# Kernel tuning notes

Measured on AMD Instinct MI355X. Metric: run time of the kernel, lower is better.

## Reference

```python
import jax, jax.numpy as jnp
import numpy as np

B = 16384      # batch
IN = 151       # input dim (layer_widths[0])
HID = 200      # RBF out_features (layer_widths[1])
CENT = 2000    # layer_centres[0]


def setup_inputs() -> dict:
    key = jax.random.key(0)
    ks = jax.random.split(key, 6)
    x = jax.random.normal(ks[0], (B, IN), dtype=jnp.float32)
    # RBF params per reset_parameters: centres ~ N(0, 0.01), sigmas = 2
    centres = 0.01 * jax.random.normal(ks[1], (HID, IN), dtype=jnp.float32)
    sigmas = jnp.full((HID,), 2.0, dtype=jnp.float32)
    # Linear layers (torch layout: weight is (out, in))
    w1 = jax.random.normal(ks[2], (CENT, HID), dtype=jnp.float32) / jnp.sqrt(jnp.float32(HID))
    b1 = jnp.zeros((CENT,), dtype=jnp.float32)
    # small scale so exp() stays well-conditioned
    w2 = 0.001 * jax.random.normal(ks[3], (CENT, CENT), dtype=jnp.float32)
    b2 = jnp.zeros((CENT,), dtype=jnp.float32)
    # kernel matrix (151, 2000); positive so Ehat[:, 0] > 0
    kern = jax.random.uniform(ks[4], (IN, CENT), dtype=jnp.float32)
    return {"x": x, "centres": centres, "sigmas": sigmas,
            "w1": w1, "b1": b1, "w2": w2, "b2": b2, "kern": kern}


def reference(x, centres, sigmas, w1, b1, w2, b2, kern):
    # RBF layer: distances_ij = ||x_i - c_j||_2 * sigma_j ; phi = exp(-distances^2)
    # exp(-(sqrt(d2)*sigma)^2) == exp(-d2 * sigma^2), so we skip the sqrt and the
    # (B, CENT, IN) expand tensor entirely.
    x2 = jnp.sum(x * x, axis=1, keepdims=True)            # (B, 1)
    c2 = jnp.sum(centres * centres, axis=1)[None, :]      # (1, HID)
    d2 = jnp.maximum(x2 + c2 - 2.0 * (x @ centres.T), 0.0)  # (B, HID)
    phi = jnp.exp(-d2 * (sigmas * sigmas)[None, :])       # (B, HID)

    h = jax.nn.relu(phi @ w1.T + b1)                      # (B, CENT)
    out = jnp.exp(h @ w2.T + b2)                          # (B, CENT)

    Ehat = out @ kern.T                                   # (B, IN)  == matmul(kern, out.T).T
    Rhat = out / Ehat[:, :1]                              # divide by correction term Ehat[:, 0]
    Ehat2 = Rhat @ kern.T                                 # (B, IN)
    return (Ehat2, Rhat, Ehat2, Rhat, x)
```

## Files before the change

kernel.cpp:

```cpp
#include <hip/hip_runtime.h>

#define BDIM 16384
#define IN_D 151
#define HID_D 200
#define CENT_D 2000

#define INP 192
#define HIDP 256
#define CENTP 2048
#define KERN_R 192

using bf16x8 = __attribute__((ext_vector_type(8))) short;
using f32x4  = __attribute__((ext_vector_type(4))) float;
using f4     = __attribute__((ext_vector_type(4))) float;
using us4    = __attribute__((ext_vector_type(4))) unsigned short;
using us8    = __attribute__((ext_vector_type(8))) unsigned short;
using i32x4  = __attribute__((ext_vector_type(4))) int;
using i32x8  = __attribute__((ext_vector_type(8))) int;

__device__ __forceinline__ unsigned short f2bf(float f) {
  unsigned u = __builtin_bit_cast(unsigned, f);
  u += 0x7FFFu + ((u >> 16) & 1u);
  return (unsigned short)(u >> 16);
}
__device__ __forceinline__ float bf2f(unsigned short h) {
  unsigned u = ((unsigned)h) << 16;
  return __builtin_bit_cast(float, u);
}
__device__ __forceinline__ unsigned char f2fp8(float f) {
  return (unsigned char)(__builtin_amdgcn_cvt_pk_fp8_f32(f, f, 0, false) & 0xFF);
}

typedef __attribute__((address_space(1))) const unsigned int guint;
typedef __attribute__((address_space(3))) unsigned int luint;
__device__ __forceinline__ void g2l16(const void* g, void* l) {
  __builtin_amdgcn_global_load_lds((guint*)g, (luint*)l, 16, 0, 0);
}

struct G0Args {
  const unsigned short* A;
  const unsigned short* B;
  const float* x2; const float* c2; const float* sg2;
  unsigned char* o8;
};

__global__ __launch_bounds__(256) void gemm_phi(G0Args p) {
  __shared__ __align__(16) short As[64 * 64];
  __shared__ __align__(16) short Bs[128 * 64];
  const int tid  = threadIdx.x;
  const int lane = tid & 63;
  const int w    = tid >> 6;
  const int wr   = w >> 1, wc = w & 1;
  const int lr   = lane & 15;
  const int tm = blockIdx.x, tn = blockIdx.y;
  f32x4 acc[2][4] = {};

  const unsigned short* Ag = p.A + (size_t)tm * 64 * INP;
  const unsigned short* Bg = p.B + (size_t)tn * 128 * INP;

  int rowa[2], cola[2], lda_[2];
#pragma unroll
  for (int i = 0; i < 2; i++) {
    int cc = i * 256 + tid;
    rowa[i] = cc >> 3;
    cola[i] = ((cc & 7) ^ (rowa[i] & 7)) * 8;
    lda_[i] = cc * 8;
  }
  int rowb[4], colb[4], ldb_[4];
#pragma unroll
  for (int i = 0; i < 4; i++) {
    int cc = i * 256 + tid;
    rowb[i] = cc >> 3;
    colb[i] = ((cc & 7) ^ (rowb[i] & 7)) * 8;
    ldb_[i] = cc * 8;
  }

  for (int k0 = 0; k0 < INP; k0 += 64) {
    __syncthreads();
#pragma unroll
    for (int i = 0; i < 2; i++)
      g2l16(Ag + (size_t)rowa[i] * INP + k0 + cola[i], &As[lda_[i]]);
#pragma unroll
    for (int i = 0; i < 4; i++)
      g2l16(Bg + (size_t)rowb[i] * INP + k0 + colb[i], &Bs[ldb_[i]]);
    __syncthreads();
#pragma unroll
    for (int ks = 0; ks < 2; ks++) {
      bf16x8 af[2], bfr[4];
#pragma unroll
      for (int m = 0; m < 2; m++) {
        int r = wr * 32 + m * 16 + lr;
        af[m] = *(const bf16x8*)&As[r * 64 + ((((ks << 2) + (lane >> 4)) ^ (r & 7)) << 3)];
      }
#pragma unroll
      for (int n = 0; n < 4; n++) {
        int r = wc * 64 + n * 16 + lr;
        bfr[n] = *(const bf16x8*)&Bs[r * 64 + ((((ks << 2) + (lane >> 4)) ^ (r & 7)) << 3)];
      }
#pragma unroll
      for (int m = 0; m < 2; m++)
#pragma unroll
        for (int n = 0; n < 4; n++)
          acc[m][n] = __builtin_amdgcn_mfma_f32_16x16x32_bf16(af[m], bfr[n], acc[m][n], 0, 0, 0);
    }
  }

  const int rb = tm * 64 + wr * 32 + (lane >> 4) * 4;
  const int cb = tn * 128 + wc * 64 + lr;
#pragma unroll
  for (int m = 0; m < 2; m++) {
#pragma unroll
    for (int n = 0; n < 4; n++) {
      const int gj = cb + n * 16;
#pragma unroll
      for (int r = 0; r < 4; r++) {
        const int gi = rb + m * 16 + r;
        float ph = 0.f;
        if (gj < HID_D) {
          float d2 = fmaxf(p.x2[gi] + p.c2[gj] - 2.f * acc[m][n][r], 0.f);
          ph = __expf(-d2 * p.sg2[gj]);
        }
        p.o8[(size_t)gi * HIDP + gj] = f2fp8(ph);
      }
    }
  }
}

struct G8Args {
  const unsigned char* A;
  const unsigned char* B;
  int K;
  const float* bias;
  unsigned short* obf;
  unsigned char* o8;
};

template<int MODE>
__global__ __launch_bounds__(256) void gemm_fp8(G8Args p) {
  __shared__ __align__(16) unsigned char As[128 * 128];
  __shared__ __align__(16) unsigned char Bs[128 * 128];
  const int tid  = threadIdx.x;
  const int lane = tid & 63;
  const int w    = tid >> 6;
  const int wr   = w >> 1, wc = w & 1;
  const int lr   = lane & 15;
  const int g    = lane >> 4;
  const int bx   = blockIdx.x;
  const int tm   = ((bx & 7) << 4) | ((bx >> 3) & 15);
  const int tn   = bx >> 7;
  const int K = p.K;
  f32x4 acc[4][4] = {};

  const unsigned char* Ag = p.A + (size_t)tm * 128 * K;
  const unsigned char* Bg = p.B + (size_t)tn * 128 * K;

  int rowc[4], colb[4], ldsb[4];
#pragma unroll
  for (int i = 0; i < 4; i++) {
    int cc = i * 256 + tid;
    rowc[i] = cc >> 3;
    colb[i] = ((cc & 7) ^ (rowc[i] & 7)) << 4;
    ldsb[i] = cc << 4;
  }

  for (int k0 = 0; k0 < K; k0 += 128) {
    __syncthreads();
#pragma unroll
    for (int i = 0; i < 4; i++)
      g2l16(Ag + (size_t)rowc[i] * K + k0 + colb[i], &As[ldsb[i]]);
#pragma unroll
    for (int i = 0; i < 4; i++)
      g2l16(Bg + (size_t)rowc[i] * K + k0 + colb[i], &Bs[ldsb[i]]);
    __syncthreads();

    i32x8 bfr[4];
#pragma unroll
    for (int n = 0; n < 4; n++) {
      const int r = wc * 64 + n * 16 + lr;
      const int rb_ = r << 7, rx = r & 7;
      i32x4 lo = *(const i32x4*)&Bs[rb_ + (((2 * g) ^ rx) << 4)];
      i32x4 hi = *(const i32x4*)&Bs[rb_ + (((2 * g + 1) ^ rx) << 4)];
      bfr[n][0] = lo[0]; bfr[n][1] = lo[1]; bfr[n][2] = lo[2]; bfr[n][3] = lo[3];
      bfr[n][4] = hi[0]; bfr[n][5] = hi[1]; bfr[n][6] = hi[2]; bfr[n][7] = hi[3];
    }
#pragma unroll
    for (int m = 0; m < 4; m++) {
      const int r = wr * 64 + m * 16 + lr;
      const int rb_ = r << 7, rx = r & 7;
      i32x4 lo = *(const i32x4*)&As[rb_ + (((2 * g) ^ rx) << 4)];
      i32x4 hi = *(const i32x4*)&As[rb_ + (((2 * g + 1) ^ rx) << 4)];
      i32x8 av;
      av[0] = lo[0]; av[1] = lo[1]; av[2] = lo[2]; av[3] = lo[3];
      av[4] = hi[0]; av[5] = hi[1]; av[6] = hi[2]; av[7] = hi[3];
#pragma unroll
      for (int n = 0; n < 4; n++)
        acc[m][n] = __builtin_amdgcn_mfma_scale_f32_16x16x128_f8f6f4(
            av, bfr[n], acc[m][n], 0, 0, 0, 127, 0, 127);
    }
  }

  const int rb = tm * 128 + wr * 64 + (lane >> 4) * 4;
  const int cb = tn * 128 + wc * 64 + lr;
  const float rs = (MODE == 1) ? 0.125f : (1.0f / 256.0f);
#pragma unroll
  for (int m = 0; m < 4; m++) {
#pragma unroll
    for (int n = 0; n < 4; n++) {
      const int gj = cb + n * 16;
      const float b = (gj < CENT_D) ? p.bias[gj] : 0.f;
#pragma unroll
      for (int r = 0; r < 4; r++) {
        const int gi = rb + m * 16 + r;
        if constexpr (MODE == 1) {
          p.o8[(size_t)gi * CENTP + gj] = f2fp8(fmaxf(acc[m][n][r] * rs + b, 0.f));
        } else {
          float o = (gj < CENT_D) ? __expf(acc[m][n][r] * rs + b) : 0.f;
          p.obf[(size_t)gi * CENTP + gj] = f2bf(o);
        }
      }
    }
  }
}

struct G3Args {
  const unsigned short* A;
  const unsigned short* B;
  float* of;
  int kspan;
};

__global__ __launch_bounds__(256, 1) void gemm3w(G3Args p) {
  __shared__ __align__(16) short As[128 * 64];
  __shared__ __align__(16) short Bs[KERN_R * 64];
  const int tid  = threadIdx.x;
  const int lane = tid & 63;
  const int w    = tid >> 6;
  const int wr   = w >> 1, wc = w & 1;
  const int lr   = lane & 15;
  const int tm = blockIdx.x;
  const int kbeg = blockIdx.y * p.kspan;
  f32x4 acc[4][6] = {};

  const unsigned short* Ag = p.A + (size_t)tm * 128 * CENTP;
  const unsigned short* Bg = p.B;

  int rowa[4], cola[4], lda_[4];
#pragma unroll
  for (int i = 0; i < 4; i++) {
    int cc = i * 256 + tid;
    rowa[i] = cc >> 3;
    cola[i] = ((cc & 7) ^ (rowa[i] & 7)) * 8;
    lda_[i] = cc * 8;
  }
  int rowb[6], colbb[6], ldb_[6];
#pragma unroll
  for (int i = 0; i < 6; i++) {
    int cc = i * 256 + tid;
    rowb[i] = cc >> 3;
    colbb[i] = ((cc & 7) ^ (rowb[i] & 7)) * 8;
    ldb_[i] = cc * 8;
  }

  for (int k0 = kbeg; k0 < kbeg + p.kspan; k0 += 64) {
    __syncthreads();
#pragma unroll
    for (int i = 0; i < 4; i++)
      g2l16(Ag + (size_t)rowa[i] * CENTP + k0 + cola[i], &As[lda_[i]]);
#pragma unroll
    for (int i = 0; i < 6; i++)
      g2l16(Bg + (size_t)rowb[i] * CENTP + k0 + colbb[i], &Bs[ldb_[i]]);
    __syncthreads();
#pragma unroll
    for (int ks = 0; ks < 2; ks++) {
      bf16x8 af[4], bfr[6];
#pragma unroll
      for (int m = 0; m < 4; m++) {
        int r = wr * 64 + m * 16 + lr;
        af[m] = *(const bf16x8*)&As[r * 64 + ((((ks << 2) + (lane >> 4)) ^ (r & 7)) << 3)];
      }
#pragma unroll
      for (int n = 0; n < 6; n++) {
        int r = wc * 96 + n * 16 + lr;
        bfr[n] = *(const bf16x8*)&Bs[r * 64 + ((((ks << 2) + (lane >> 4)) ^ (r & 7)) << 3)];
      }
#pragma unroll
      for (int m = 0; m < 4; m++)
#pragma unroll
        for (int n = 0; n < 6; n++)
          acc[m][n] = __builtin_amdgcn_mfma_f32_16x16x32_bf16(af[m], bfr[n], acc[m][n], 0, 0, 0);
    }
  }

  float* of = p.of + (size_t)blockIdx.y * BDIM * IN_D;
  const int rb = tm * 128 + wr * 64 + (lane >> 4) * 4;
  const int cb = wc * 96 + lr;
#pragma unroll
  for (int m = 0; m < 4; m++) {
#pragma unroll
    for (int n = 0; n < 6; n++) {
      const int gj = cb + n * 16;
#pragma unroll
      for (int r = 0; r < 4; r++) {
        const int gi = rb + m * 16 + r;
        if (gj < IN_D) of[(size_t)gi * IN_D + gj] = acc[m][n][r];
      }
    }
  }
}

#define NB_CAST 3504
#define NB_LOWP 4608
#define NB_MISC 4161

__global__ __launch_bounds__(256) void prep_all(
    const float* __restrict__ x, const float* __restrict__ cen,
    const float* __restrict__ kern, const float* __restrict__ w1,
    const float* __restrict__ w2, const float* __restrict__ sg,
    unsigned short* __restrict__ x_bf, unsigned short* __restrict__ c_bf,
    unsigned short* __restrict__ kernp, unsigned char* __restrict__ w1p8,
    unsigned char* __restrict__ w2p8, float* __restrict__ x2,
    float* __restrict__ c2, float* __restrict__ sg2,
    float* __restrict__ xo) {
  const int b = blockIdx.x;
  if (b < NB_CAST) {
    const int c = b * 256 + threadIdx.x;
    const float* src; unsigned short* dst; int R, C, cpq, local, vec, isx;
    if (c < 786432)      { src = x;    dst = x_bf;  R = 16384; C = 151;  cpq = 48;  local = c;           vec = 0; isx = 1; }
    else if (c < 798720) { src = cen;  dst = c_bf;  R = 200;   C = 151;  cpq = 48;  local = c - 786432;  vec = 0; isx = 0; }
    else                 { src = kern; dst = kernp; R = 151;   C = 2000; cpq = 512; local = c - 798720;  vec = 1; isx = 0; }
    const int r  = local / cpq;
    const int c4 = (local - r * cpq) << 2;
    us4 o;
    if (vec && r < R && c4 + 3 < C) {
      f4 v = *(const f4*)&src[(size_t)r * C + c4];
      o[0] = f2bf(v[0]); o[1] = f2bf(v[1]); o[2] = f2bf(v[2]); o[3] = f2bf(v[3]);
    } else {
#pragma unroll
      for (int k = 0; k < 4; k++) {
        float v = (r < R && c4 + k < C) ? src[(size_t)r * C + c4 + k] : 0.f;
        o[k] = f2bf(v);
        if (isx && c4 + k < C) xo[(size_t)r * IN_D + c4 + k] = v;
      }
    }
    *(us4*)&dst[(size_t)local * 4] = o;
  } else if (b < NB_CAST + NB_LOWP) {
    const int i = (b - NB_CAST) * 256 + threadIdx.x;
    const float* src; unsigned char* dst; int r, c4, R, C; float sc;
    int j;
    if (i < 131072) { src = w1; dst = w1p8; j = i;          r = j >> 6; c4 = (j & 63) << 2;  R = 2000; C = 200;  sc = 8.f; }
    else            { src = w2; dst = w2p8; j = i - 131072; r = j >> 9; c4 = (j & 511) << 2; R = 2000; C = 2000; sc = 256.f; }
    float v[4];
#pragma unroll
    for (int k = 0; k < 4; k++)
      v[k] = (r < R && c4 + k < C) ? src[(size_t)r * C + c4 + k] * sc : 0.f;
    int p0 = __builtin_amdgcn_cvt_pk_fp8_f32(v[0], v[1], 0, false);
    int p1 = __builtin_amdgcn_cvt_pk_fp8_f32(v[2], v[3], 0, false);
    *(unsigned int*)&dst[(size_t)j * 4] =
        ((unsigned)p0 & 0xFFFFu) | (((unsigned)p1 & 0xFFFFu) << 16);
  } else {
    const int b2 = b - NB_CAST - NB_LOWP;
    if (b2 == 4160) {
      int j = threadIdx.x;
      sg2[j] = (j < HID_D) ? sg[j] * sg[j] : 0.f;
      return;
    }
    const float* src; float* dst; int R, base;
    if (b2 < 4096) { src = x;   dst = x2; R = BDIM;  base = b2 * 4; }
    else           { src = cen; dst = c2; R = HID_D; base = (b2 - 4096) * 4; }
    const int row = base + (threadIdx.x >> 6);
    const int l = threadIdx.x & 63;
    float s = 0.f;
    if (row < R)
      for (int k = l; k < IN_D; k += 64) { float v = src[(size_t)row * IN_D + k]; s += v * v; }
#pragma unroll
    for (int off = 32; off > 0; off >>= 1) s += __shfl_down(s, off);
    if (l == 0) dst[row] = s;
  }
}

__global__ __launch_bounds__(256) void finalize(
    float* __restrict__ dout, const unsigned short* __restrict__ outp,
    const float* __restrict__ part) {
  const int i = blockIdx.x;
  const size_t SL = (size_t)BDIM * IN_D;
  float* Eh = dout;
  float* Ra = dout + SL;
  float* Eb = dout + SL + (size_t)BDIM * CENT_D;
  float* Rb = Eb + SL;
  const size_t ib = (size_t)i * IN_D;
  const float e0 = part[ib] + part[SL + ib];
  const float s = 1.f / e0;
  const int t = threadIdx.x;
  if (t < IN_D) {
    float v = (part[ib + t] + part[SL + ib + t]) * s;
    Eh[ib + t] = v;
    Eb[ib + t] = v;
  }
  if (t < 250) {
    const us8 u = *(const us8*)&outp[(size_t)i * CENTP + t * 8];
    f4 a, b;
#pragma unroll
    for (int k = 0; k < 4; k++) a[k] = bf2f(u[k]) * s;
#pragma unroll
    for (int k = 0; k < 4; k++) b[k] = bf2f(u[4 + k]) * s;
    const size_t o = (size_t)i * CENT_D + t * 8;
    *(f4*)&Ra[o] = a; *(f4*)&Ra[o + 4] = b;
    *(f4*)&Rb[o] = a; *(f4*)&Rb[o + 4] = b;
  }
}

extern "C" void kernel_launch(void* const* d_in, const int* in_sizes, int n_in,
                              void* d_out, int out_size, void* d_ws, size_t ws_size,
                              hipStream_t stream) {
  (void)in_sizes; (void)n_in; (void)out_size; (void)ws_size;
  const float* x       = (const float*)d_in[0];
  const float* centres = (const float*)d_in[1];
  const float* sigmas  = (const float*)d_in[2];
  const float* w1      = (const float*)d_in[3];
  const float* b1      = (const float*)d_in[4];
  const float* w2      = (const float*)d_in[5];
  const float* b2      = (const float*)d_in[6];
  const float* kern    = (const float*)d_in[7];
  float* dout = (float*)d_out;

  char* ws = (char*)d_ws;
  size_t off = 0;
  auto alloc = [&](size_t bytes) {
    char* p = ws + off;
    off = (off + bytes + 255) & ~(size_t)255;
    return p;
  };
  unsigned short* x_bf  = (unsigned short*)alloc((size_t)BDIM * INP * 2);
  unsigned short* c_bf  = (unsigned short*)alloc((size_t)256 * INP * 2);
  unsigned char*  w1p8  = (unsigned char*)alloc((size_t)CENTP * HIDP);
  unsigned char*  w2p8  = (unsigned char*)alloc((size_t)CENTP * CENTP);
  unsigned short* kernp = (unsigned short*)alloc((size_t)KERN_R * CENTP * 2);
  unsigned char*  phip8 = (unsigned char*)alloc((size_t)BDIM * HIDP);
  unsigned short* outp  = (unsigned short*)alloc((size_t)BDIM * CENTP * 2);
  float* x2  = (float*)alloc((size_t)BDIM * 4);
  float* c2  = (float*)alloc((size_t)256 * 4);
  float* sg2 = (float*)alloc((size_t)256 * 4);
  float* eparts = (float*)alloc((size_t)2 * BDIM * IN_D * 4);
  unsigned char* hp8 = (unsigned char*)(dout + (size_t)BDIM * (2 * IN_D + CENT_D));
  float* xo = dout + (size_t)BDIM * (2 * IN_D + 2 * CENT_D);

  prep_all<<<NB_CAST + NB_LOWP + NB_MISC, 256, 0, stream>>>(
      x, centres, kern, w1, w2, sigmas,
      x_bf, c_bf, kernp, w1p8, w2p8, x2, c2, sg2, xo);

  G0Args g0{}; g0.A = x_bf; g0.B = c_bf;
  g0.x2 = x2; g0.c2 = c2; g0.sg2 = sg2; g0.o8 = phip8;
  gemm_phi<<<dim3(BDIM / 64, HIDP / 128), 256, 0, stream>>>(g0);

  G8Args g1{}; g1.A = phip8; g1.B = w1p8; g1.K = HIDP;
  g1.bias = b1; g1.o8 = hp8;
  gemm_fp8<1><<<2048, 256, 0, stream>>>(g1);

  G8Args g2{}; g2.A = hp8; g2.B = w2p8; g2.K = CENTP;
  g2.bias = b2; g2.obf = outp;
  gemm_fp8<2><<<2048, 256, 0, stream>>>(g2);

  G3Args g3{}; g3.A = outp; g3.B = kernp; g3.of = eparts; g3.kspan = CENTP / 2;
  gemm3w<<<dim3(BDIM / 128, 2), 256, 0, stream>>>(g3);

  finalize<<<BDIM, 256, 0, stream>>>(dout, outp, eparts);
}
```

Measured before the change: 225.5 us.

## Store exp output in FP8 and run final kernel GEMM with FP8 MFMA

```diff
diff --git a/kernel.cpp b/kernel.cpp
--- a/kernel.cpp
+++ b/kernel.cpp
@@ -14,7 +14,6 @@
 using f32x4  = __attribute__((ext_vector_type(4))) float;
 using f4     = __attribute__((ext_vector_type(4))) float;
 using us4    = __attribute__((ext_vector_type(4))) unsigned short;
-using us8    = __attribute__((ext_vector_type(8))) unsigned short;
 using i32x4  = __attribute__((ext_vector_type(4))) int;
 using i32x8  = __attribute__((ext_vector_type(8))) int;
 
@@ -23,12 +22,15 @@
   u += 0x7FFFu + ((u >> 16) & 1u);
   return (unsigned short)(u >> 16);
 }
-__device__ __forceinline__ float bf2f(unsigned short h) {
-  unsigned u = ((unsigned)h) << 16;
-  return __builtin_bit_cast(float, u);
-}
 __device__ __forceinline__ unsigned char f2fp8(float f) {
   return (unsigned char)(__builtin_amdgcn_cvt_pk_fp8_f32(f, f, 0, false) & 0xFF);
+}
+__device__ __forceinline__ float fp8d(unsigned b) {
+  unsigned s = b >> 7, e = (b >> 3) & 15, m = b & 7;
+  unsigned fb = (s << 31) | ((e + 120) << 23) | (m << 20);
+  float nrm = __builtin_bit_cast(float, fb);
+  float sub = (s ? -1.f : 1.f) * (float)m * 0.001953125f;
+  return e ? nrm : sub;
 }
 
 typedef __attribute__((address_space(1))) const unsigned int guint;
@@ -131,7 +133,6 @@
   const unsigned char* B;
   int K;
   const float* bias;
-  unsigned short* obf;
   unsigned char* o8;
 };
 
@@ -215,7 +216,7 @@
           p.o8[(size_t)gi * CENTP + gj] = f2fp8(fmaxf(acc[m][n][r] * rs + b, 0.f));
         } else {
           float o = (gj < CENT_D) ? __expf(acc[m][n][r] * rs + b) : 0.f;
-          p.obf[(size_t)gi * CENTP + gj] = f2bf(o);
+          p.o8[(size_t)gi * CENTP + gj] = f2fp8(o);
         }
       }
     }
@@ -223,93 +224,97 @@
 }
 
 struct G3Args {
-  const unsigned short* A;
-  const unsigned short* B;
-  float* of;
-  int kspan;
+  const unsigned char* A;
+  const unsigned char* B;
+  float* eh;
 };
 
-__global__ __launch_bounds__(256, 1) void gemm3w(G3Args p) {
-  __shared__ __align__(16) short As[128 * 64];
-  __shared__ __align__(16) short Bs[KERN_R * 64];
+__global__ __launch_bounds__(256) void gemm3f8(G3Args p) {
+  __shared__ __align__(16) unsigned char As[64 * 128];
+  __shared__ __align__(16) unsigned char Bs[KERN_R * 128];
   const int tid  = threadIdx.x;
   const int lane = tid & 63;
   const int w    = tid >> 6;
   const int wr   = w >> 1, wc = w & 1;
   const int lr   = lane & 15;
+  const int g    = lane >> 4;
   const int tm = blockIdx.x;
-  const int kbeg = blockIdx.y * p.kspan;
-  f32x4 acc[4][6] = {};
-
-  const unsigned short* Ag = p.A + (size_t)tm * 128 * CENTP;
-  const unsigned short* Bg = p.B;
-
-  int rowa[4], cola[4], lda_[4];
-#pragma unroll
-  for (int i = 0; i < 4; i++) {
+  f32x4 acc[2][6] = {};
+
+  const unsigned char* Ag = p.A + (size_t)tm * 64 * CENTP;
+  const unsigned char* Bg = p.B;
+
+  int rowa[2], cola[2], lda_[2];
+#pragma unroll
+  for (int i = 0; i < 2; i++) {
     int cc = i * 256 + tid;
     rowa[i] = cc >> 3;
-    cola[i] = ((cc & 7) ^ (rowa[i] & 7)) * 8;
-    lda_[i] = cc * 8;
+    cola[i] = ((cc & 7) ^ (rowa[i] & 7)) << 4;
+    lda_[i] = cc << 4;
   }
   int rowb[6], colbb[6], ldb_[6];
 #pragma unroll
   for (int i = 0; i < 6; i++) {
     int cc = i * 256 + tid;
     rowb[i] = cc >> 3;
-    colbb[i] = ((cc & 7) ^ (rowb[i] & 7)) * 8;
-    ldb_[i] = cc * 8;
-  }
-
-  for (int k0 = kbeg; k0 < kbeg + p.kspan; k0 += 64) {
-    __syncthreads();
-#pragma unroll
-    for (int i = 0; i < 4; i++)
+    colbb[i] = ((cc & 7) ^ (rowb[i] & 7)) << 4;
+    ldb_[i] = cc << 4;
+  }
+
+  for (int k0 = 0; k0 < CENTP; k0 += 128) {
+    __syncthreads();
+#pragma unroll
+    for (int i = 0; i < 2; i++)
       g2l16(Ag + (size_t)rowa[i] * CENTP + k0 + cola[i], &As[lda_[i]]);
 #pragma unroll
     for (int i = 0; i < 6; i++)
       g2l16(Bg + (size_t)rowb[i] * CENTP + k0 + colbb[i], &Bs[ldb_[i]]);
     __syncthreads();
-#pragma unroll
-    for (int ks = 0; ks < 2; ks++) {
-      bf16x8 af[4], bfr[6];
-#pragma unroll
-      for (int m = 0; m < 4; m++) {
-        int r = wr * 64 + m * 16 + lr;
-        af[m] = *(const bf16x8*)&As[r * 64 + ((((ks << 2) + (lane >> 4)) ^ (r & 7)) << 3)];
-      }
-#pragma unroll
-      for (int n = 0; n < 6; n++) {
-        int r = wc * 96 + n * 16 + lr;
-        bfr[n] = *(const bf16x8*)&Bs[r * 64 + ((((ks << 2) + (lane >> 4)) ^ (r & 7)) << 3)];
-      }
-#pragma unroll
-      for (int m = 0; m < 4; m++)
-#pragma unroll
-        for (int n = 0; n < 6; n++)
-          acc[m][n] = __builtin_amdgcn_mfma_f32_16x16x32_bf16(af[m], bfr[n], acc[m][n], 0, 0, 0);
-    }
-  }
-
-  float* of = p.of + (size_t)blockIdx.y * BDIM * IN_D;
-  const int rb = tm * 128 + wr * 64 + (lane >> 4) * 4;
+
+    i32x8 bfr[6];
+#pragma unroll
+    for (int n = 0; n < 6; n++) {
+      const int r = wc * 96 + n * 16 + lr;
+      const int rb_ = r << 7, rx = r & 7;
+      i32x4 lo = *(const i32x4*)&Bs[rb_ + (((2 * g) ^ rx) << 4)];
+      i32x4 hi = *(const i32x4*)&Bs[rb_ + (((2 * g + 1) ^ rx) << 4)];
+      bfr[n][0] = lo[0]; bfr[n][1] = lo[1]; bfr[n][2] = lo[2]; bfr[n][3] = lo[3];
+      bfr[n][4] = hi[0]; bfr[n][5] = hi[1]; bfr[n][6] = hi[2]; bfr[n][7] = hi[3];
+    }
+#pragma unroll
+    for (int m = 0; m < 2; m++) {
+      const int r = wr * 32 + m * 16 + lr;
+      const int rb_ = r << 7, rx = r & 7;
+      i32x4 lo = *(const i32x4*)&As[rb_ + (((2 * g) ^ rx) << 4)];
+      i32x4 hi = *(const i32x4*)&As[rb_ + (((2 * g + 1) ^ rx) << 4)];
+      i32x8 av;
+      av[0] = lo[0]; av[1] = lo[1]; av[2] = lo[2]; av[3] = lo[3];
+      av[4] = hi[0]; av[5] = hi[1]; av[6] = hi[2]; av[7] = hi[3];
+#pragma unroll
+      for (int n = 0; n < 6; n++)
+        acc[m][n] = __builtin_amdgcn_mfma_scale_f32_16x16x128_f8f6f4(
+            av, bfr[n], acc[m][n], 0, 0, 0, 127, 0, 127);
+    }
+  }
+
+  const int rb = tm * 64 + wr * 32 + (lane >> 4) * 4;
   const int cb = wc * 96 + lr;
 #pragma unroll
-  for (int m = 0; m < 4; m++) {
+  for (int m = 0; m < 2; m++) {
 #pragma unroll
     for (int n = 0; n < 6; n++) {
       const int gj = cb + n * 16;
 #pragma unroll
       for (int r = 0; r < 4; r++) {
         const int gi = rb + m * 16 + r;
-        if (gj < IN_D) of[(size_t)gi * IN_D + gj] = acc[m][n][r];
+        if (gj < IN_D) p.eh[(size_t)gi * IN_D + gj] = acc[m][n][r];
       }
     }
   }
 }
 
-#define NB_CAST 3504
-#define NB_LOWP 4608
+#define NB_CAST 3120
+#define NB_LOWP 4992
 #define NB_MISC 4161
 
 __global__ __launch_bounds__(256) void prep_all(
@@ -317,38 +322,34 @@
     const float* __restrict__ kern, const float* __restrict__ w1,
     const float* __restrict__ w2, const float* __restrict__ sg,
     unsigned short* __restrict__ x_bf, unsigned short* __restrict__ c_bf,
-    unsigned short* __restrict__ kernp, unsigned char* __restrict__ w1p8,
+    unsigned char* __restrict__ kernp8, unsigned char* __restrict__ w1p8,
     unsigned char* __restrict__ w2p8, float* __restrict__ x2,
     float* __restrict__ c2, float* __restrict__ sg2,
     float* __restrict__ xo) {
   const int b = blockIdx.x;
   if (b < NB_CAST) {
     const int c = b * 256 + threadIdx.x;
-    const float* src; unsigned short* dst; int R, C, cpq, local, vec, isx;
-    if (c < 786432)      { src = x;    dst = x_bf;  R = 16384; C = 151;  cpq = 48;  local = c;           vec = 0; isx = 1; }
-    else if (c < 798720) { src = cen;  dst = c_bf;  R = 200;   C = 151;  cpq = 48;  local = c - 786432;  vec = 0; isx = 0; }
-    else                 { src = kern; dst = kernp; R = 151;   C = 2000; cpq = 512; local = c - 798720;  vec = 1; isx = 0; }
-    const int r  = local / cpq;
-    const int c4 = (local - r * cpq) << 2;
+    const float* src; unsigned short* dst; int local, isx;
+    if (c < 786432) { src = x;   dst = x_bf; local = c;          isx = 1; }
+    else            { src = cen; dst = c_bf; local = c - 786432; isx = 0; }
+    const int R = isx ? BDIM : 200;
+    const int r  = local / 48;
+    const int c4 = (local - r * 48) << 2;
     us4 o;
-    if (vec && r < R && c4 + 3 < C) {
-      f4 v = *(const f4*)&src[(size_t)r * C + c4];
-      o[0] = f2bf(v[0]); o[1] = f2bf(v[1]); o[2] = f2bf(v[2]); o[3] = f2bf(v[3]);
-    } else {
-#pragma unroll
-      for (int k = 0; k < 4; k++) {
-        float v = (r < R && c4 + k < C) ? src[(size_t)r * C + c4 + k] : 0.f;
-        o[k] = f2bf(v);
-        if (isx && c4 + k < C) xo[(size_t)r * IN_D + c4 + k] = v;
-      }
+#pragma unroll
+    for (int k = 0; k < 4; k++) {
+      float v = (r < R && c4 + k < IN_D) ? src[(size_t)r * IN_D + c4 + k] : 0.f;
+      o[k] = f2bf(v);
+      if (isx && c4 + k < IN_D) xo[(size_t)r * IN_D + c4 + k] = v;
     }
     *(us4*)&dst[(size_t)local * 4] = o;
   } else if (b < NB_CAST + NB_LOWP) {
     const int i = (b - NB_CAST) * 256 + threadIdx.x;
     const float* src; unsigned char* dst; int r, c4, R, C; float sc;
     int j;
-    if (i < 131072) { src = w1; dst = w1p8; j = i;          r = j >> 6; c4 = (j & 63) << 2;  R = 2000; C = 200;  sc = 8.f; }
-    else            { src = w2; dst = w2p8; j = i - 131072; r = j >> 9; c4 = (j & 511) << 2; R = 2000; C = 2000; sc = 256.f; }
+    if (i < 131072)       { src = w1;   dst = w1p8;   j = i;           r = j >> 6; c4 = (j & 63) << 2;  R = 2000; C = 200;  sc = 8.f; }
+    else if (i < 1179648) { src = w2;   dst = w2p8;   j = i - 131072;  r = j >> 9; c4 = (j & 511) << 2; R = 2000; C = 2000; sc = 256.f; }
+    else                  { src = kern; dst = kernp8; j = i - 1179648; r = j >> 9; c4 = (j & 511) << 2; R = 151;  C = 2000; sc = 1.f; }
     float v[4];
 #pragma unroll
     for (int k = 0; k < 4; k++)
@@ -379,8 +380,7 @@
 }
 
 __global__ __launch_bounds__(256) void finalize(
-    float* __restrict__ dout, const unsigned short* __restrict__ outp,
-    const float* __restrict__ part) {
+    float* __restrict__ dout, const unsigned char* __restrict__ outp8) {
   const int i = blockIdx.x;
   const size_t SL = (size_t)BDIM * IN_D;
   float* Eh = dout;
@@ -388,21 +388,22 @@
   float* Eb = dout + SL + (size_t)BDIM * CENT_D;
   float* Rb = Eb + SL;
   const size_t ib = (size_t)i * IN_D;
-  const float e0 = part[ib] + part[SL + ib];
+  const float e0 = Eh[ib];
+  __syncthreads();
   const float s = 1.f / e0;
   const int t = threadIdx.x;
   if (t < IN_D) {
-    float v = (part[ib + t] + part[SL + ib + t]) * s;
+    float v = Eh[ib + t] * s;
     Eh[ib + t] = v;
     Eb[ib + t] = v;
   }
   if (t < 250) {
-    const us8 u = *(const us8*)&outp[(size_t)i * CENTP + t * 8];
+    unsigned long long v = *(const unsigned long long*)&outp8[(size_t)i * CENTP + t * 8];
     f4 a, b;
 #pragma unroll
-    for (int k = 0; k < 4; k++) a[k] = bf2f(u[k]) * s;
-#pragma unroll
-    for (int k = 0; k < 4; k++) b[k] = bf2f(u[4 + k]) * s;
+    for (int k = 0; k < 4; k++) a[k] = fp8d((unsigned)(v >> (8 * k)) & 0xFFu) * s;
+#pragma unroll
+    for (int k = 0; k < 4; k++) b[k] = fp8d((unsigned)(v >> (8 * (k + 4))) & 0xFFu) * s;
     const size_t o = (size_t)i * CENT_D + t * 8;
     *(f4*)&Ra[o] = a; *(f4*)&Ra[o + 4] = b;
     *(f4*)&Rb[o] = a; *(f4*)&Rb[o + 4] = b;
@@ -434,19 +435,18 @@
   unsigned short* c_bf  = (unsigned short*)alloc((size_t)256 * INP * 2);
   unsigned char*  w1p8  = (unsigned char*)alloc((size_t)CENTP * HIDP);
   unsigned char*  w2p8  = (unsigned char*)alloc((size_t)CENTP * CENTP);
-  unsigned short* kernp = (unsigned short*)alloc((size_t)KERN_R * CENTP * 2);
+  unsigned char*  kernp8= (unsigned char*)alloc((size_t)KERN_R * CENTP);
   unsigned char*  phip8 = (unsigned char*)alloc((size_t)BDIM * HIDP);
-  unsigned short* outp  = (unsigned short*)alloc((size_t)BDIM * CENTP * 2);
+  unsigned char*  outp8 = (unsigned char*)alloc((size_t)BDIM * CENTP);
   float* x2  = (float*)alloc((size_t)BDIM * 4);
   float* c2  = (float*)alloc((size_t)256 * 4);
   float* sg2 = (float*)alloc((size_t)256 * 4);
-  float* eparts = (float*)alloc((size_t)2 * BDIM * IN_D * 4);
   unsigned char* hp8 = (unsigned char*)(dout + (size_t)BDIM * (2 * IN_D + CENT_D));
   float* xo = dout + (size_t)BDIM * (2 * IN_D + 2 * CENT_D);
 
   prep_all<<<NB_CAST + NB_LOWP + NB_MISC, 256, 0, stream>>>(
       x, centres, kern, w1, w2, sigmas,
-      x_bf, c_bf, kernp, w1p8, w2p8, x2, c2, sg2, xo);
+      x_bf, c_bf, kernp8, w1p8, w2p8, x2, c2, sg2, xo);
 
   G0Args g0{}; g0.A = x_bf; g0.B = c_bf;
   g0.x2 = x2; g0.c2 = c2; g0.sg2 = sg2; g0.o8 = phip8;
@@ -457,11 +457,11 @@
   gemm_fp8<1><<<2048, 256, 0, stream>>>(g1);
 
   G8Args g2{}; g2.A = hp8; g2.B = w2p8; g2.K = CENTP;
-  g2.bias = b2; g2.obf = outp;
+  g2.bias = b2; g2.o8 = outp8;
   gemm_fp8<2><<<2048, 256, 0, stream>>>(g2);
 
-  G3Args g3{}; g3.A = outp; g3.B = kernp; g3.of = eparts; g3.kspan = CENTP / 2;
-  gemm3w<<<dim3(BDIM / 128, 2), 256, 0, stream>>>(g3);
-
-  finalize<<<BDIM, 256, 0, stream>>>(dout, outp, eparts);
-}
+  G3Args g3{}; g3.A = outp8; g3.B = kernp8; g3.eh = dout;
+  gemm3f8<<<256, 256, 0, stream>>>(g3);
+
+  finalize<<<BDIM, 256, 0, stream>>>(dout, outp8);
+}
```

Result: slower. 236.1 us (+4.7%).
